# Optimization experiments

Measured on AMD Instinct MI355X. Metric: run time of the kernel, lower is better.

The kernel has to match this reference:

```python
import jax, jax.numpy as jnp
import numpy as np

N, DIM, T, V = 32, 256, 120, 25
H, HD = 8, 32            # num_heads, head_dim
MAX_HOP = 4
SCALE = HD ** -0.5


def setup_inputs() -> dict:
    key = jax.random.key(0)
    ks = jax.random.split(key, 9)
    x = jax.random.normal(ks[0], (N, DIM, T, V), jnp.float32)
    e = jax.random.normal(ks[1], (N, DIM, T, V), jnp.float32)
    # 1x1 conv weights (trunc_normal std=0.02 in the original init)
    W_kv = jax.random.normal(ks[2], (2 * DIM, DIM), jnp.float32) * 0.02
    W_q = jax.random.normal(ks[3], (DIM, DIM), jnp.float32) * 0.02
    W_proj = jax.random.normal(ks[4], (DIM, DIM), jnp.float32) * 0.02
    b_proj = jnp.zeros((DIM,), jnp.float32)
    rpe = jax.random.normal(ks[5], (MAX_HOP + 1, DIM), jnp.float32) * 0.02
    w1 = jax.random.normal(ks[6], (H, HD), jnp.float32) * 0.02
    # outer initialized as per-head identity (plus noise so grads are interesting)
    outer = jnp.broadcast_to(jnp.eye(V, dtype=jnp.float32), (H, V, V)) \
        + 0.1 * jax.random.normal(ks[7], (H, V, V), jnp.float32)
    alpha = 0.1 * jax.random.normal(ks[8], (1,), jnp.float32)
    idx = jnp.arange(V)
    hops = jnp.minimum(jnp.abs(idx[:, None] - idx[None, :]), MAX_HOP).astype(jnp.int32)
    return dict(x=x, e=e, W_kv=W_kv, W_q=W_q, W_proj=W_proj, b_proj=b_proj,
                rpe=rpe, w1=w1, outer=outer, alpha=alpha, hops=hops)


def reference(x, e, W_kv, W_q, W_proj, b_proj, rpe, w1, outer, alpha, hops):
    n, c, t, v = x.shape
    # 1x1 convs == channel matmuls
    kv = jnp.einsum('nctv,dc->ndtv', x, W_kv)                    # [N,2*DIM,T,V]
    kv = kv.reshape(n, 2, H, HD, t, v).transpose(1, 0, 4, 2, 5, 3)  # [2,N,T,H,V,HD]
    k, vv = kv[0], kv[1]
    q = jnp.einsum('nctv,dc->ndtv', x, W_q)
    q = q.reshape(n, H, HD, t, v).transpose(0, 3, 1, 4, 2)       # [N,T,H,V,HD]
    # content score
    attn = jnp.einsum('bthnc,bthmc->bthnm', q, k)                # [N,T,H,V,V]
    # hop relative-position bias
    k_r = rpe[hops].reshape(v, v, H, HD)                         # [V,V,H,HD]
    attn = attn + jnp.einsum('bthnc,nmhc->bthnm', q, k_r)
    # group term
    e_k = e.reshape(n, H, HD, t, v).transpose(0, 3, 1, 4, 2)     # [N,T,H,V,HD]
    attn = attn + jnp.einsum('bthnc,bthmc->bthnm', q, e_k)
    # group bias (broadcast over query index)
    attn = attn + jnp.einsum('hc,bthmc->bthm', w1, e_k)[..., None, :]
    attn = jax.nn.softmax(attn * SCALE, axis=-1)
    # outer/adjacency fusion then weighted V
    out = jnp.einsum('bthnm,bthmc->bthnc', alpha[0] * attn + outer, vv)
    # [N,T,H,V,HD] -> [N,T,H,HD,V] -> [N,T,DIM,V] -> [N,DIM,T,V]
    out = out.transpose(0, 1, 2, 4, 3).reshape(n, t, H * HD, v).transpose(0, 2, 1, 3)
    out = jnp.einsum('nctv,dc->ndtv', out, W_proj) + b_proj[None, :, None, None]
    return out
```

## Files before the change

### kernel.cpp

```cpp
#include <hip/hip_runtime.h>

typedef __attribute__((ext_vector_type(8))) short bf16x8;
typedef __attribute__((ext_vector_type(4))) float f32x4;
typedef unsigned short u16;
typedef unsigned int u32;

#define SCALE_ 0.17677669529663687f
#define MFMA(a,b,c) __builtin_amdgcn_mfma_f32_16x16x32_bf16(a,b,c,0,0,0)

__device__ __forceinline__ u16 f2bf(float f){
    u32 u = __float_as_uint(f);
    u = (u + 0x7FFFu + ((u >> 16) & 1u)) >> 16;
    return (u16)u;
}
__device__ __forceinline__ float bf2f(u32 h){ return __uint_as_float(h << 16); }
__device__ __forceinline__ u32 pk2(float a, float b){ return (u32)f2bf(a) | ((u32)f2bf(b) << 16); }

__device__ __forceinline__ bf16x8 frag8(uint2 p0, uint2 p1, int kg, int l15){
    const int s0 = ((kg & 1) << 5) + l15;
    const int s1 = s0 + 16;
    u32 a0 = (u32)__shfl((int)p0.x, s0, 64);
    u32 a1 = (u32)__shfl((int)p0.y, s0, 64);
    u32 a2 = (u32)__shfl((int)p0.x, s1, 64);
    u32 a3 = (u32)__shfl((int)p0.y, s1, 64);
    u32 b0 = (u32)__shfl((int)p1.x, s0, 64);
    u32 b1 = (u32)__shfl((int)p1.y, s0, 64);
    u32 b2 = (u32)__shfl((int)p1.x, s1, 64);
    u32 b3 = (u32)__shfl((int)p1.y, s1, 64);
    const bool hi = (kg >= 2);
    union { u32 u[4]; bf16x8 v; } r;
    r.u[0] = hi ? b0 : a0; r.u[1] = hi ? b1 : a1;
    r.u[2] = hi ? b2 : a2; r.u[3] = hi ? b3 : a3;
    return r.v;
}

#define O_OFF_ 263680
__global__ void prep_kernel(const float* __restrict__ Wkv, const float* __restrict__ Wq,
                            const float* __restrict__ Wproj, const float* __restrict__ rpe,
                            const float* __restrict__ w1, u16* __restrict__ wpk)
{
    int i = blockIdx.x * 256 + threadIdx.x;
    if (i < 65536)        wpk[i] = f2bf(Wq[i]);
    else if (i < 131072)  wpk[i] = f2bf(Wkv[i - 65536]);
    else if (i < 196608){
        int j = i - 131072;
        int h = j >> 13;
        int r = j & 8191;
        int coct = r >> 8;
        int hd   = (r >> 3) & 31;
        int clo  = r & 7;
        wpk[i] = f2bf(Wkv[(size_t)(256 + h*32 + hd) * 256 + coct*8 + clo]);
    }
    else if (i < 262144)  wpk[i] = f2bf(Wproj[i - 196608]);
    else if (i < 263424){
        int j = i - 262144;
        int jj = j >> 8, h = (j >> 5) & 7, hd = j & 31;
        wpk[i] = f2bf(rpe[jj*256 + h*32 + hd]);
    }
    else if (i < 263680)  wpk[i] = f2bf(w1[i - 263424]);
}

__launch_bounds__(512)
__global__ void attn_kernel(const float* __restrict__ x, const float* __restrict__ e,
                            const float* __restrict__ outer, const float* __restrict__ alpha,
                            const u16* __restrict__ wpk, u16* __restrict__ o_ws)
{
    __shared__ __align__(16) u16 smem[6656*2 + 64];
    u16* xs  = smem;
    u16* es  = smem + 6656;

    const int tid = threadIdx.x;
    const int w = tid >> 6, lane = tid & 63;
    const int l15 = lane & 15, kg = lane >> 4;
    const int wg = (blockIdx.x & 7) * 480 + (blockIdx.x >> 3);
    const int n = wg / 120, t = wg % 120;
    const float alpha0 = alpha[0];
    const f32x4 zf = {0.f, 0.f, 0.f, 0.f};

    const float* xb = x + (size_t)n*768000 + t*25;
    const float* eb = e + (size_t)n*768000 + t*25;
    for (int i = tid; i < 6400; i += 512){
        int c = i / 25, v = i - c*25;
        int a16 = ((c>>3)*26 + v)*8 + (c&7);
        xs[a16] = f2bf(xb[c*3000 + v]);
        es[a16] = f2bf(eb[c*3000 + v]);
    }
    __syncthreads();

    const int h = w;

    f32x4 cq[2][2], ck[2][2];
    #pragma unroll
    for (int i = 0; i < 2; ++i)
        #pragma unroll
        for (int j = 0; j < 2; ++j){ cq[i][j] = zf; ck[i][j] = zf; }
    {
        const u16* wq0 = wpk + (size_t)(h*32 + l15)*256;
        const u16* wk0 = wpk + 65536 + (size_t)(h*32 + l15)*256;
        #pragma unroll
        for (int ks = 0; ks < 8; ++ks){
            bf16x8 b0 = *(const bf16x8*)&xs[((ks*4+kg)*26 + l15)*8];
            bf16x8 b1 = *(const bf16x8*)&xs[((ks*4+kg)*26 + 16 + l15)*8];
            bf16x8 aq0 = *(const bf16x8*)(wq0 + ks*32 + kg*8);
            bf16x8 aq1 = *(const bf16x8*)(wq0 + 4096 + ks*32 + kg*8);
            bf16x8 ak0 = *(const bf16x8*)(wk0 + ks*32 + kg*8);
            bf16x8 ak1 = *(const bf16x8*)(wk0 + 4096 + ks*32 + kg*8);
            cq[0][0]=MFMA(aq0,b0,cq[0][0]); cq[0][1]=MFMA(aq0,b1,cq[0][1]);
            cq[1][0]=MFMA(aq1,b0,cq[1][0]); cq[1][1]=MFMA(aq1,b1,cq[1][1]);
            ck[0][0]=MFMA(ak0,b0,ck[0][0]); ck[0][1]=MFMA(ak0,b1,ck[0][1]);
            ck[1][0]=MFMA(ak1,b0,ck[1][0]); ck[1][1]=MFMA(ak1,b1,ck[1][1]);
        }
    }
    uint2 P_q[2][2], P_k[2][2];
    #pragma unroll
    for (int mt = 0; mt < 2; ++mt)
        #pragma unroll
        for (int nt = 0; nt < 2; ++nt){
            int coct = h*4 + mt*2 + (kg>>1);
            uint2 ev = *(const uint2*)&es[(coct*26 + nt*16 + l15)*8 + (kg&1)*4];
            ck[mt][nt][0] += bf2f(ev.x & 0xFFFFu);
            ck[mt][nt][1] += bf2f(ev.x >> 16);
            ck[mt][nt][2] += bf2f(ev.y & 0xFFFFu);
            ck[mt][nt][3] += bf2f(ev.y >> 16);
            uint2 pq; pq.x = pk2(cq[mt][nt][0], cq[mt][nt][1]);
            pq.y = pk2(cq[mt][nt][2], cq[mt][nt][3]);
            P_q[nt][mt] = pq;
            uint2 pk; pk.x = pk2(ck[mt][nt][0], ck[mt][nt][1]);
            pk.y = pk2(ck[mt][nt][2], ck[mt][nt][3]);
            P_k[nt][mt] = pk;
        }

    float bias01[2];
    {
        bf16x8 aw1 = *(const bf16x8*)(wpk + 263424 + h*32 + kg*8);
        bf16x8 be0 = *(const bf16x8*)&es[((h*4+kg)*26 + l15)*8];
        bf16x8 be1 = *(const bf16x8*)&es[((h*4+kg)*26 + 16 + l15)*8];
        f32x4 cb0 = MFMA(aw1, be0, zf);
        f32x4 cb1 = MFMA(aw1, be1, zf);
        bias01[0] = cb0[0]; bias01[1] = cb1[0];
    }

    f32x4 cv[2][2];
    #pragma unroll
    for (int i = 0; i < 2; ++i)
        #pragma unroll
        for (int j = 0; j < 2; ++j) cv[i][j] = zf;
    {
        const u16* wvt = wpk + 131072 + h*8192;
        #pragma unroll
        for (int ks = 0; ks < 8; ++ks){
            bf16x8 a0 = *(const bf16x8*)&xs[((ks*4+kg)*26 + l15)*8];
            bf16x8 a1 = *(const bf16x8*)&xs[((ks*4+kg)*26 + 16 + l15)*8];
            bf16x8 bv0 = *(const bf16x8*)&wvt[((ks*4+kg)*32 + l15)*8];
            bf16x8 bv1 = *(const bf16x8*)&wvt[((ks*4+kg)*32 + 16 + l15)*8];
            cv[0][0]=MFMA(a0,bv0,cv[0][0]); cv[0][1]=MFMA(a0,bv1,cv[0][1]);
            cv[1][0]=MFMA(a1,bv0,cv[1][0]); cv[1][1]=MFMA(a1,bv1,cv[1][1]);
        }
    }
    #pragma unroll
    for (int nt = 0; nt < 2; ++nt)
        #pragma unroll
        for (int r = 0; r < 4; ++r)
            cv[1][nt][r] = (kg*4 + r < 9) ? cv[1][nt][r] : 0.f;

    uint2 P_v[2][2];
    #pragma unroll
    for (int mt = 0; mt < 2; ++mt)
        #pragma unroll
        for (int nt = 0; nt < 2; ++nt){
            uint2 pv; pv.x = pk2(cv[mt][nt][0], cv[mt][nt][1]);
            pv.y = pk2(cv[mt][nt][2], cv[mt][nt][3]);
            P_v[nt][mt] = pv;
        }

    bf16x8 fq0  = frag8(P_q[0][0], P_q[0][1], kg, l15);
    bf16x8 fq1  = frag8(P_q[1][0], P_q[1][1], kg, l15);
    bf16x8 fke0 = frag8(P_k[0][0], P_k[0][1], kg, l15);
    bf16x8 fke1 = frag8(P_k[1][0], P_k[1][1], kg, l15);
    if (l15 >= 9){
        if (l15 <= 13)
            fke1 = *(const bf16x8*)(wpk + 262144 + ((l15-9)*8 + h)*32 + kg*8);
        else {
            union { u32 u[4]; bf16x8 v; } z; z.u[0]=z.u[1]=z.u[2]=z.u[3]=0;
            fke1 = z.v;
        }
    }
    f32x4 sc[2][2];
    sc[0][0] = MFMA(fke0, fq0, zf);
    sc[0][1] = MFMA(fke0, fq1, zf);
    sc[1][0] = MFMA(fke1, fq0, zf);
    sc[1][1] = MFMA(fke1, fq1, zf);

    uint2 P_G[2][2];
    #pragma unroll
    for (int nt = 0; nt < 2; ++nt){
        const int a = nt*16 + l15;
        f32x4 s0 = sc[0][nt], s1 = sc[1][nt];
        float rr0 = __shfl(s1[1], 32 + l15, 64);
        float rr1 = __shfl(s1[2], 32 + l15, 64);
        float rr2 = __shfl(s1[3], 32 + l15, 64);
        float rr3 = __shfl(s1[0], 48 + l15, 64);
        float rr4 = __shfl(s1[1], 48 + l15, 64);
        float tv[8];
        #pragma unroll
        for (int mt = 0; mt < 2; ++mt)
            #pragma unroll
            for (int r = 0; r < 4; ++r){
                int b = mt*16 + kg*4 + r;
                float sval = mt ? s1[r] : s0[r];
                float bb = __shfl(bias01[mt], (lane & 48) + (b & 15), 64);
                int d = a - b; d = d < 0 ? -d : d; if (d > 4) d = 4;
                float rj = d==0?rr0 : d==1?rr1 : d==2?rr2 : d==3?rr3 : rr4;
                float tt = (sval + rj + bb) * SCALE_;
                tv[mt*4+r] = (b < 25) ? tt : -1e30f;
            }
        float m = tv[0];
        #pragma unroll
        for (int i = 1; i < 8; ++i) m = fmaxf(m, tv[i]);
        m = fmaxf(m, __shfl_xor(m, 16, 64));
        m = fmaxf(m, __shfl_xor(m, 32, 64));
        float ex[8], sm = 0.f;
        #pragma unroll
        for (int i = 0; i < 8; ++i){ ex[i] = __expf(tv[i] - m); sm += ex[i]; }
        sm += __shfl_xor(sm, 16, 64);
        sm += __shfl_xor(sm, 32, 64);
        const float inv = alpha0 / sm;
        float g[8];
        #pragma unroll
        for (int mt = 0; mt < 2; ++mt)
            #pragma unroll
            for (int r = 0; r < 4; ++r){
                int b = mt*16 + kg*4 + r;
                float ov = (a < 25 && b < 25) ? outer[((size_t)h*25 + a)*25 + b] : 0.f;
                g[mt*4+r] = (b < 25) ? ex[mt*4+r]*inv + ov : 0.f;
            }
        uint2 pg0; pg0.x = pk2(g[0], g[1]); pg0.y = pk2(g[2], g[3]);
        uint2 pg1; pg1.x = pk2(g[4], g[5]); pg1.y = pk2(g[6], g[7]);
        P_G[nt][0] = pg0; P_G[nt][1] = pg1;
    }

    {
        bf16x8 fv0 = frag8(P_v[0][0], P_v[0][1], kg, l15);
        bf16x8 fv1 = frag8(P_v[1][0], P_v[1][1], kg, l15);
        bf16x8 fg0 = frag8(P_G[0][0], P_G[0][1], kg, l15);
        bf16x8 fg1 = frag8(P_G[1][0], P_G[1][1], kg, l15);
        f32x4 o[2][2];
        o[0][0] = MFMA(fv0, fg0, zf); o[0][1] = MFMA(fv0, fg1, zf);
        o[1][0] = MFMA(fv1, fg0, zf); o[1][1] = MFMA(fv1, fg1, zf);
        u16* od = o_ws + (size_t)wg * 6400;
        #pragma unroll
        for (int mt = 0; mt < 2; ++mt)
            #pragma unroll
            for (int nt = 0; nt < 2; ++nt){
                int a = nt*16 + l15;
                if (a < 25){
                    int coct = h*4 + mt*2 + (kg>>1);
                    u32* dst = (u32*)&od[(coct*25 + a)*8 + (kg&1)*4];
                    dst[0] = pk2(o[mt][nt][0], o[mt][nt][1]);
                    dst[1] = pk2(o[mt][nt][2], o[mt][nt][3]);
                }
            }
    }
}

__launch_bounds__(512)
__global__ void proj_kernel(const u16* __restrict__ wpk, const u16* __restrict__ o_ws,
                            const float* __restrict__ bproj, float* __restrict__ out)
{
    const int tid = threadIdx.x;
    const int w = tid >> 6, lane = tid & 63;
    const int l15 = lane & 15, kg = lane >> 4;
    const int wg = (blockIdx.x & 7) * 480 + (blockIdx.x >> 3);
    const int n = wg / 120, t = wg % 120;
    const f32x4 zf = {0.f, 0.f, 0.f, 0.f};
    const u16* ob = o_ws + (size_t)wg * 6400;

    f32x4 pc[2][2];
    #pragma unroll
    for (int i = 0; i < 2; ++i){ pc[i][0] = zf; pc[i][1] = zf; }
    #pragma unroll
    for (int ks = 0; ks < 8; ++ks){
        bf16x8 pb0 = *(const bf16x8*)&ob[((ks*4+kg)*25 + l15)*8];
        bf16x8 pb1 = *(const bf16x8*)&ob[((ks*4+kg)*25 + 16 + l15)*8];
        #pragma unroll
        for (int i = 0; i < 2; ++i){
            bf16x8 aw = *(const bf16x8*)(wpk + 196608 +
                            (size_t)(w*32 + i*16 + l15)*256 + ks*32 + kg*8);
            pc[i][0] = MFMA(aw, pb0, pc[i][0]);
            pc[i][1] = MFMA(aw, pb1, pc[i][1]);
        }
    }
    #pragma unroll
    for (int i = 0; i < 2; ++i){
        const int d = w*32 + i*16 + kg*4;
        float b0 = bproj[d], b1 = bproj[d+1], b2 = bproj[d+2], b3 = bproj[d+3];
        #pragma unroll
        for (int nt = 0; nt < 2; ++nt){
            int v = nt*16 + l15;
            if (v < 25){
                float* op = out + (size_t)n*768000 + (size_t)d*3000 + t*25 + v;
                op[0]    = pc[i][nt][0] + b0;
                op[3000] = pc[i][nt][1] + b1;
                op[6000] = pc[i][nt][2] + b2;
                op[9000] = pc[i][nt][3] + b3;
            }
        }
    }
}

__launch_bounds__(512, 4)
__global__ void mhsa_main(const float* __restrict__ x, const float* __restrict__ e,
                          const float* __restrict__ outer, const float* __restrict__ alpha,
                          const float* __restrict__ bproj, const u16* __restrict__ wpk,
                          float* __restrict__ out)
{
    __shared__ __align__(16) u16 smem[6656*3 + 64];
    u16* xs  = smem;
    u16* es  = smem + 6656;
    u16* opk = smem + 13312;

    const int tid = threadIdx.x;
    const int w = tid >> 6, lane = tid & 63;
    const int l15 = lane & 15, kg = lane >> 4;
    const int wg = (blockIdx.x & 7) * 480 + (blockIdx.x >> 3);
    const int n = wg / 120, t = wg % 120;
    const float alpha0 = alpha[0];
    const f32x4 zf = {0.f, 0.f, 0.f, 0.f};

    const float* xb = x + (size_t)n*768000 + t*25;
    const float* eb = e + (size_t)n*768000 + t*25;
    for (int i = tid; i < 6400; i += 512){
        int c = i / 25, v = i - c*25;
        int a16 = ((c>>3)*26 + v)*8 + (c&7);
        xs[a16] = f2bf(xb[c*3000 + v]);
        es[a16] = f2bf(eb[c*3000 + v]);
    }
    __syncthreads();

    {
        const int h = w;
        f32x4 cq[2][2], ck[2][2];
        #pragma unroll
        for (int i = 0; i < 2; ++i)
            #pragma unroll
            for (int j = 0; j < 2; ++j){ cq[i][j] = zf; ck[i][j] = zf; }
        {
            const u16* wq0 = wpk + (size_t)(h*32 + l15)*256;
            const u16* wk0 = wpk + 65536 + (size_t)(h*32 + l15)*256;
            #pragma unroll
            for (int ks = 0; ks < 8; ++ks){
                bf16x8 b0 = *(const bf16x8*)&xs[((ks*4+kg)*26 + l15)*8];
                bf16x8 b1 = *(const bf16x8*)&xs[((ks*4+kg)*26 + 16 + l15)*8];
                bf16x8 aq0 = *(const bf16x8*)(wq0 + ks*32 + kg*8);
                bf16x8 aq1 = *(const bf16x8*)(wq0 + 4096 + ks*32 + kg*8);
                bf16x8 ak0 = *(const bf16x8*)(wk0 + ks*32 + kg*8);
                bf16x8 ak1 = *(const bf16x8*)(wk0 + 4096 + ks*32 + kg*8);
                cq[0][0]=MFMA(aq0,b0,cq[0][0]); cq[0][1]=MFMA(aq0,b1,cq[0][1]);
                cq[1][0]=MFMA(aq1,b0,cq[1][0]); cq[1][1]=MFMA(aq1,b1,cq[1][1]);
                ck[0][0]=MFMA(ak0,b0,ck[0][0]); ck[0][1]=MFMA(ak0,b1,ck[0][1]);
                ck[1][0]=MFMA(ak1,b0,ck[1][0]); ck[1][1]=MFMA(ak1,b1,ck[1][1]);
            }
        }
        uint2 P_q[2][2], P_k[2][2];
        #pragma unroll
        for (int mt = 0; mt < 2; ++mt)
            #pragma unroll
            for (int nt = 0; nt < 2; ++nt){
                int coct = h*4 + mt*2 + (kg>>1);
                uint2 ev = *(const uint2*)&es[(coct*26 + nt*16 + l15)*8 + (kg&1)*4];
                ck[mt][nt][0] += bf2f(ev.x & 0xFFFFu);
                ck[mt][nt][1] += bf2f(ev.x >> 16);
                ck[mt][nt][2] += bf2f(ev.y & 0xFFFFu);
                ck[mt][nt][3] += bf2f(ev.y >> 16);
                uint2 pq; pq.x = pk2(cq[mt][nt][0], cq[mt][nt][1]);
                pq.y = pk2(cq[mt][nt][2], cq[mt][nt][3]);
                P_q[nt][mt] = pq;
                uint2 pk; pk.x = pk2(ck[mt][nt][0], ck[mt][nt][1]);
                pk.y = pk2(ck[mt][nt][2], ck[mt][nt][3]);
                P_k[nt][mt] = pk;
            }
        float bias01[2];
        {
            bf16x8 aw1 = *(const bf16x8*)(wpk + 263424 + h*32 + kg*8);
            bf16x8 be0 = *(const bf16x8*)&es[((h*4+kg)*26 + l15)*8];
            bf16x8 be1 = *(const bf16x8*)&es[((h*4+kg)*26 + 16 + l15)*8];
            f32x4 cb0 = MFMA(aw1, be0, zf);
            f32x4 cb1 = MFMA(aw1, be1, zf);
            bias01[0] = cb0[0]; bias01[1] = cb1[0];
        }
        f32x4 cv[2][2];
        #pragma unroll
        for (int i = 0; i < 2; ++i)
            #pragma unroll
            for (int j = 0; j < 2; ++j) cv[i][j] = zf;
        {
            const u16* wvt = wpk + 131072 + h*8192;
            #pragma unroll
            for (int ks = 0; ks < 8; ++ks){
                bf16x8 a0 = *(const bf16x8*)&xs[((ks*4+kg)*26 + l15)*8];
                bf16x8 a1 = *(const bf16x8*)&xs[((ks*4+kg)*26 + 16 + l15)*8];
                bf16x8 bv0 = *(const bf16x8*)&wvt[((ks*4+kg)*32 + l15)*8];
                bf16x8 bv1 = *(const bf16x8*)&wvt[((ks*4+kg)*32 + 16 + l15)*8];
                cv[0][0]=MFMA(a0,bv0,cv[0][0]); cv[0][1]=MFMA(a0,bv1,cv[0][1]);
                cv[1][0]=MFMA(a1,bv0,cv[1][0]); cv[1][1]=MFMA(a1,bv1,cv[1][1]);
            }
        }
        #pragma unroll
        for (int nt = 0; nt < 2; ++nt)
            #pragma unroll
            for (int r = 0; r < 4; ++r)
                cv[1][nt][r] = (kg*4 + r < 9) ? cv[1][nt][r] : 0.f;
        uint2 P_v[2][2];
        #pragma unroll
        for (int mt = 0; mt < 2; ++mt)
            #pragma unroll
            for (int nt = 0; nt < 2; ++nt){
                uint2 pv; pv.x = pk2(cv[mt][nt][0], cv[mt][nt][1]);
                pv.y = pk2(cv[mt][nt][2], cv[mt][nt][3]);
                P_v[nt][mt] = pv;
            }
        bf16x8 fq0  = frag8(P_q[0][0], P_q[0][1], kg, l15);
        bf16x8 fq1  = frag8(P_q[1][0], P_q[1][1], kg, l15);
        bf16x8 fke0 = frag8(P_k[0][0], P_k[0][1], kg, l15);
        bf16x8 fke1 = frag8(P_k[1][0], P_k[1][1], kg, l15);
        if (l15 >= 9){
            if (l15 <= 13)
                fke1 = *(const bf16x8*)(wpk + 262144 + ((l15-9)*8 + h)*32 + kg*8);
            else {
                union { u32 u[4]; bf16x8 v; } z; z.u[0]=z.u[1]=z.u[2]=z.u[3]=0;
                fke1 = z.v;
            }
        }
        f32x4 sc[2][2];
        sc[0][0] = MFMA(fke0, fq0, zf);
        sc[0][1] = MFMA(fke0, fq1, zf);
        sc[1][0] = MFMA(fke1, fq0, zf);
        sc[1][1] = MFMA(fke1, fq1, zf);
        uint2 P_G[2][2];
        #pragma unroll
        for (int nt = 0; nt < 2; ++nt){
            const int a = nt*16 + l15;
            f32x4 s0 = sc[0][nt], s1 = sc[1][nt];
            float rr0 = __shfl(s1[1], 32 + l15, 64);
            float rr1 = __shfl(s1[2], 32 + l15, 64);
            float rr2 = __shfl(s1[3], 32 + l15, 64);
            float rr3 = __shfl(s1[0], 48 + l15, 64);
            float rr4 = __shfl(s1[1], 48 + l15, 64);
            float tv[8];
            #pragma unroll
            for (int mt = 0; mt < 2; ++mt)
                #pragma unroll
                for (int r = 0; r < 4; ++r){
                    int b = mt*16 + kg*4 + r;
                    float sval = mt ? s1[r] : s0[r];
                    float bb = __shfl(bias01[mt], (lane & 48) + (b & 15), 64);
                    int d = a - b; d = d < 0 ? -d : d; if (d > 4) d = 4;
                    float rj = d==0?rr0 : d==1?rr1 : d==2?rr2 : d==3?rr3 : rr4;
                    float tt = (sval + rj + bb) * SCALE_;
                    tv[mt*4+r] = (b < 25) ? tt : -1e30f;
                }
            float m = tv[0];
            #pragma unroll
            for (int i = 1; i < 8; ++i) m = fmaxf(m, tv[i]);
            m = fmaxf(m, __shfl_xor(m, 16, 64));
            m = fmaxf(m, __shfl_xor(m, 32, 64));
            float ex[8], sm = 0.f;
            #pragma unroll
            for (int i = 0; i < 8; ++i){ ex[i] = __expf(tv[i] - m); sm += ex[i]; }
            sm += __shfl_xor(sm, 16, 64);
            sm += __shfl_xor(sm, 32, 64);
            const float inv = alpha0 / sm;
            float g[8];
            #pragma unroll
            for (int mt = 0; mt < 2; ++mt)
                #pragma unroll
                for (int r = 0; r < 4; ++r){
                    int b = mt*16 + kg*4 + r;
                    float ov = (a < 25 && b < 25) ? outer[((size_t)h*25 + a)*25 + b] : 0.f;
                    g[mt*4+r] = (b < 25) ? ex[mt*4+r]*inv + ov : 0.f;
                }
            uint2 pg0; pg0.x = pk2(g[0], g[1]); pg0.y = pk2(g[2], g[3]);
            uint2 pg1; pg1.x = pk2(g[4], g[5]); pg1.y = pk2(g[6], g[7]);
            P_G[nt][0] = pg0; P_G[nt][1] = pg1;
        }
        {
            bf16x8 fv0 = frag8(P_v[0][0], P_v[0][1], kg, l15);
            bf16x8 fv1 = frag8(P_v[1][0], P_v[1][1], kg, l15);
            bf16x8 fg0 = frag8(P_G[0][0], P_G[0][1], kg, l15);
            bf16x8 fg1 = frag8(P_G[1][0], P_G[1][1], kg, l15);
            f32x4 o[2][2];
            o[0][0] = MFMA(fv0, fg0, zf); o[0][1] = MFMA(fv0, fg1, zf);
            o[1][0] = MFMA(fv1, fg0, zf); o[1][1] = MFMA(fv1, fg1, zf);
            #pragma unroll
            for (int mt = 0; mt < 2; ++mt)
                #pragma unroll
                for (int nt = 0; nt < 2; ++nt){
                    int a = nt*16 + l15;
                    if (a < 25){
                        int coct = h*4 + mt*2 + (kg>>1);
                        u32* dst = (u32*)&opk[(coct*26 + a)*8 + (kg&1)*4];
                        dst[0] = pk2(o[mt][nt][0], o[mt][nt][1]);
                        dst[1] = pk2(o[mt][nt][2], o[mt][nt][3]);
                    }
                }
        }
    }
    __syncthreads();

    {
        f32x4 pc[2][2];
        #pragma unroll
        for (int i = 0; i < 2; ++i){ pc[i][0] = zf; pc[i][1] = zf; }
        #pragma unroll
        for (int ks = 0; ks < 8; ++ks){
            bf16x8 pb0 = *(const bf16x8*)&opk[((ks*4+kg)*26 + l15)*8];
            bf16x8 pb1 = *(const bf16x8*)&opk[((ks*4+kg)*26 + 16 + l15)*8];
            #pragma unroll
            for (int i = 0; i < 2; ++i){
                bf16x8 aw = *(const bf16x8*)(wpk + 196608 +
                                (size_t)(w*32 + i*16 + l15)*256 + ks*32 + kg*8);
                pc[i][0] = MFMA(aw, pb0, pc[i][0]);
                pc[i][1] = MFMA(aw, pb1, pc[i][1]);
            }
        }
        #pragma unroll
        for (int i = 0; i < 2; ++i){
            const int d = w*32 + i*16 + kg*4;
            float b0 = bproj[d], b1 = bproj[d+1], b2 = bproj[d+2], b3 = bproj[d+3];
            #pragma unroll
            for (int nt = 0; nt < 2; ++nt){
                int v = nt*16 + l15;
                if (v < 25){
                    float* op = out + (size_t)n*768000 + (size_t)d*3000 + t*25 + v;
                    op[0]    = pc[i][nt][0] + b0;
                    op[3000] = pc[i][nt][1] + b1;
                    op[6000] = pc[i][nt][2] + b2;
                    op[9000] = pc[i][nt][3] + b3;
                }
            }
        }
    }
}

extern "C" void kernel_launch(void* const* d_in, const int* in_sizes, int n_in,
                              void* d_out, int out_size, void* d_ws, size_t ws_size,
                              hipStream_t stream) {
    (void)in_sizes; (void)n_in; (void)out_size;
    const float* x     = (const float*)d_in[0];
    const float* e     = (const float*)d_in[1];
    const float* Wkv   = (const float*)d_in[2];
    const float* Wq    = (const float*)d_in[3];
    const float* Wproj = (const float*)d_in[4];
    const float* bproj = (const float*)d_in[5];
    const float* rpe   = (const float*)d_in[6];
    const float* w1    = (const float*)d_in[7];
    const float* outer = (const float*)d_in[8];
    const float* alpha = (const float*)d_in[9];
    float* out = (float*)d_out;
    u16* wpk = (u16*)d_ws;

    prep_kernel<<<1030, 256, 0, stream>>>(Wkv, Wq, Wproj, rpe, w1, wpk);

    const size_t need = (size_t)O_OFF_*2 + (size_t)3840*6400*2 + 4096;
    if (ws_size >= need){
        u16* o_ws = wpk + O_OFF_;
        attn_kernel<<<32*120, 512, 0, stream>>>(x, e, outer, alpha, wpk, o_ws);
        proj_kernel<<<32*120, 512, 0, stream>>>(wpk, o_ws, bproj, out);
    } else {
        mhsa_main<<<32*120, 512, 0, stream>>>(x, e, outer, alpha, bproj, wpk, out);
    }
}
```

Measured before the change: 315.2 us.

## Split QKV projection into a batched GEMM kernel and fuse attention with output projection

Moves the Q, K and V 1x1-conv projections into a separate GEMM kernel. Each block handles one projection section over four time steps (100 columns), so weight fragments are reused across more columns and x and e are loaded with float4 reads. The result is written as per-(n,t,head) bf16 pages already laid out as MFMA fragments, plus a precomputed group-bias buffer. Attention and the output projection are fused into one kernel through shared memory, replacing the old global o_ws round trip. The cost is extra global traffic for the Q/K/V pages and the bias buffer, and a larger workspace requirement.

```diff
diff --git a/kernel.cpp b/kernel.cpp
--- a/kernel.cpp
+++ b/kernel.cpp
@@ -34,23 +34,17 @@
     return r.v;
 }
 
-#define O_OFF_ 263680
+#define PG_OFF_ 333312
+#define NPAGES_ ((size_t)3840*8*2624)
+#define BIAS_U16_ (PG_OFF_ + NPAGES_)
+
 __global__ void prep_kernel(const float* __restrict__ Wkv, const float* __restrict__ Wq,
                             const float* __restrict__ Wproj, const float* __restrict__ rpe,
                             const float* __restrict__ w1, u16* __restrict__ wpk)
 {
     int i = blockIdx.x * 256 + threadIdx.x;
     if (i < 65536)        wpk[i] = f2bf(Wq[i]);
-    else if (i < 131072)  wpk[i] = f2bf(Wkv[i - 65536]);
-    else if (i < 196608){
-        int j = i - 131072;
-        int h = j >> 13;
-        int r = j & 8191;
-        int coct = r >> 8;
-        int hd   = (r >> 3) & 31;
-        int clo  = r & 7;
-        wpk[i] = f2bf(Wkv[(size_t)(256 + h*32 + hd) * 256 + coct*8 + clo]);
-    }
+    else if (i < 196608)  wpk[i] = f2bf(Wkv[i - 65536]);
     else if (i < 262144)  wpk[i] = f2bf(Wproj[i - 196608]);
     else if (i < 263424){
         int j = i - 262144;
@@ -58,138 +52,184 @@
         wpk[i] = f2bf(rpe[jj*256 + h*32 + hd]);
     }
     else if (i < 263680)  wpk[i] = f2bf(w1[i - 263424]);
+    else if (i < 267776){
+        int j = i - 263680;
+        int r = j >> 8, c = j & 255;
+        float v = (r < 8 && (c >> 5) == r) ? w1[r*32 + (c & 31)] : 0.f;
+        wpk[i] = f2bf(v);
+    }
+    else if (i < 333312){
+        int j = i - 267776;
+        int h = j >> 13;
+        int r = j & 8191;
+        int coct = r >> 8, hd = (r >> 3) & 31, clo = r & 7;
+        wpk[i] = f2bf(Wkv[(size_t)(256 + h*32 + hd) * 256 + coct*8 + clo]);
+    }
 }
 
 __launch_bounds__(512)
-__global__ void attn_kernel(const float* __restrict__ x, const float* __restrict__ e,
-                            const float* __restrict__ outer, const float* __restrict__ alpha,
-                            const u16* __restrict__ wpk, u16* __restrict__ o_ws)
+__global__ void qkv_gemm(const float* __restrict__ x, const float* __restrict__ e,
+                         const u16* __restrict__ wpk, u16* __restrict__ pages,
+                         float* __restrict__ bias_ws)
 {
-    __shared__ __align__(16) u16 smem[6656*2 + 64];
-    u16* xs  = smem;
-    u16* es  = smem + 6656;
+    __shared__ __align__(16) u16 xt[25664];
 
     const int tid = threadIdx.x;
     const int w = tid >> 6, lane = tid & 63;
     const int l15 = lane & 15, kg = lane >> 4;
-    const int wg = (blockIdx.x & 7) * 480 + (blockIdx.x >> 3);
+    const int wg = ((int)blockIdx.x & 7) * 360 + ((int)blockIdx.x >> 3);
+    const int sec = wg / 960, cb = wg % 960;
+    const int n = cb / 30, tg = cb % 30;
+    const f32x4 zf = {0.f, 0.f, 0.f, 0.f};
+
+    const float* xb = x + (size_t)n*768000 + tg*100;
+    for (int i = tid; i < 6400; i += 512){
+        int c = i / 25, c4 = i - c*25;
+        float4 v4 = *(const float4*)&xb[c*3000 + c4*4];
+        int base = ((c>>3)*100 + c4*4)*8 + (c&7);
+        xt[base]    = f2bf(v4.x);
+        xt[base+8]  = f2bf(v4.y);
+        xt[base+16] = f2bf(v4.z);
+        xt[base+24] = f2bf(v4.w);
+    }
+    __syncthreads();
+
+    f32x4 acc[2][8];
+    #pragma unroll
+    for (int m = 0; m < 2; ++m)
+        #pragma unroll
+        for (int f = 0; f < 8; ++f) acc[m][f] = zf;
+
+    const u16* wrow = wpk + (size_t)(sec*256 + w*32 + l15) * 256;
+    #pragma unroll
+    for (int ks = 0; ks < 8; ++ks){
+        bf16x8 a0 = *(const bf16x8*)(wrow + ks*32 + kg*8);
+        bf16x8 a1 = *(const bf16x8*)(wrow + 4096 + ks*32 + kg*8);
+        #pragma unroll
+        for (int f = 0; f < 8; ++f){
+            int col = (f>>1)*25 + (f&1)*16 + l15;
+            bf16x8 b = *(const bf16x8*)&xt[((ks*4+kg)*100 + col)*8];
+            acc[0][f] = MFMA(a0, b, acc[0][f]);
+            acc[1][f] = MFMA(a1, b, acc[1][f]);
+        }
+    }
+
+    if (sec == 1){
+        __syncthreads();
+        const float* ebp = e + (size_t)n*768000 + tg*100;
+        for (int i = tid; i < 6400; i += 512){
+            int c = i / 25, c4 = i - c*25;
+            float4 v4 = *(const float4*)&ebp[c*3000 + c4*4];
+            int base = ((c>>3)*100 + c4*4)*8 + (c&7);
+            xt[base]    = f2bf(v4.x);
+            xt[base+8]  = f2bf(v4.y);
+            xt[base+16] = f2bf(v4.z);
+            xt[base+24] = f2bf(v4.w);
+        }
+        __syncthreads();
+        #pragma unroll
+        for (int m = 0; m < 2; ++m){
+            int c0 = w*32 + m*16 + kg*4;
+            #pragma unroll
+            for (int f = 0; f < 8; ++f){
+                int col = (f>>1)*25 + (f&1)*16 + l15;
+                uint2 ev = *(const uint2*)&xt[((c0>>3)*100 + col)*8 + (c0&7)];
+                acc[m][f][0] += bf2f(ev.x & 0xFFFFu);
+                acc[m][f][1] += bf2f(ev.x >> 16);
+                acc[m][f][2] += bf2f(ev.y & 0xFFFFu);
+                acc[m][f][3] += bf2f(ev.y >> 16);
+            }
+        }
+    }
+
+    const int secoff = (sec == 0) ? 0 : (sec == 1 ? 800 : 1600);
+    #pragma unroll
+    for (int m = 0; m < 2; ++m){
+        #pragma unroll
+        for (int f = 0; f < 8; ++f){
+            int tt = f >> 1, a = (f&1)*16 + l15;
+            if (a < 25){
+                size_t nt = (size_t)(n*120 + tg*4 + tt);
+                u16* pg = pages + (nt*8 + w)*2624 + secoff;
+                int hd0 = m*16 + kg*4;
+                if (sec < 2){
+                    uint2 val; val.x = pk2(acc[m][f][0], acc[m][f][1]);
+                    val.y = pk2(acc[m][f][2], acc[m][f][3]);
+                    *(uint2*)&pg[((hd0>>3)*25 + a)*8 + (hd0&7)] = val;
+                } else {
+                    #pragma unroll
+                    for (int r = 0; r < 4; ++r)
+                        pg[((a>>3)*32 + hd0 + r)*8 + (a&7)] = f2bf(acc[m][f][r]);
+                }
+            }
+        }
+    }
+
+    if (sec == 1 && w == 0){
+        f32x4 bacc[8];
+        #pragma unroll
+        for (int f = 0; f < 8; ++f) bacc[f] = zf;
+        const u16* w1f = wpk + 263680 + l15*256;
+        #pragma unroll
+        for (int ks = 0; ks < 8; ++ks){
+            bf16x8 a = *(const bf16x8*)(w1f + ks*32 + kg*8);
+            #pragma unroll
+            for (int f = 0; f < 8; ++f){
+                int col = (f>>1)*25 + (f&1)*16 + l15;
+                bf16x8 b = *(const bf16x8*)&xt[((ks*4+kg)*100 + col)*8];
+                bacc[f] = MFMA(a, b, bacc[f]);
+            }
+        }
+        if (kg < 2){
+            #pragma unroll
+            for (int f = 0; f < 8; ++f){
+                int tt = f >> 1, a = (f&1)*16 + l15;
+                if (a < 25){
+                    int nt = n*120 + tg*4 + tt;
+                    #pragma unroll
+                    for (int r = 0; r < 4; ++r)
+                        bias_ws[(size_t)nt*256 + (kg*4+r)*32 + a] = bacc[f][r];
+                }
+            }
+        }
+    }
+}
+
+__launch_bounds__(512)
+__global__ void attn_proj(const float* __restrict__ outer, const float* __restrict__ alpha,
+                          const float* __restrict__ bproj, const u16* __restrict__ wpk,
+                          const u16* __restrict__ pages, const float* __restrict__ bias_ws,
+                          float* __restrict__ out)
+{
+    __shared__ __align__(16) u16 opk[6656 + 64];
+
+    const int tid = threadIdx.x;
+    const int w = tid >> 6, lane = tid & 63;
+    const int l15 = lane & 15, kg = lane >> 4;
+    const int wg = ((int)blockIdx.x & 7) * 480 + ((int)blockIdx.x >> 3);
     const int n = wg / 120, t = wg % 120;
     const float alpha0 = alpha[0];
     const f32x4 zf = {0.f, 0.f, 0.f, 0.f};
-
-    const float* xb = x + (size_t)n*768000 + t*25;
-    const float* eb = e + (size_t)n*768000 + t*25;
-    for (int i = tid; i < 6400; i += 512){
-        int c = i / 25, v = i - c*25;
-        int a16 = ((c>>3)*26 + v)*8 + (c&7);
-        xs[a16] = f2bf(xb[c*3000 + v]);
-        es[a16] = f2bf(eb[c*3000 + v]);
-    }
-    __syncthreads();
-
     const int h = w;
-
-    f32x4 cq[2][2], ck[2][2];
-    #pragma unroll
-    for (int i = 0; i < 2; ++i)
-        #pragma unroll
-        for (int j = 0; j < 2; ++j){ cq[i][j] = zf; ck[i][j] = zf; }
-    {
-        const u16* wq0 = wpk + (size_t)(h*32 + l15)*256;
-        const u16* wk0 = wpk + 65536 + (size_t)(h*32 + l15)*256;
-        #pragma unroll
-        for (int ks = 0; ks < 8; ++ks){
-            bf16x8 b0 = *(const bf16x8*)&xs[((ks*4+kg)*26 + l15)*8];
-            bf16x8 b1 = *(const bf16x8*)&xs[((ks*4+kg)*26 + 16 + l15)*8];
-            bf16x8 aq0 = *(const bf16x8*)(wq0 + ks*32 + kg*8);
-            bf16x8 aq1 = *(const bf16x8*)(wq0 + 4096 + ks*32 + kg*8);
-            bf16x8 ak0 = *(const bf16x8*)(wk0 + ks*32 + kg*8);
-            bf16x8 ak1 = *(const bf16x8*)(wk0 + 4096 + ks*32 + kg*8);
-            cq[0][0]=MFMA(aq0,b0,cq[0][0]); cq[0][1]=MFMA(aq0,b1,cq[0][1]);
-            cq[1][0]=MFMA(aq1,b0,cq[1][0]); cq[1][1]=MFMA(aq1,b1,cq[1][1]);
-            ck[0][0]=MFMA(ak0,b0,ck[0][0]); ck[0][1]=MFMA(ak0,b1,ck[0][1]);
-            ck[1][0]=MFMA(ak1,b0,ck[1][0]); ck[1][1]=MFMA(ak1,b1,ck[1][1]);
-        }
-    }
-    uint2 P_q[2][2], P_k[2][2];
-    #pragma unroll
-    for (int mt = 0; mt < 2; ++mt)
-        #pragma unroll
-        for (int nt = 0; nt < 2; ++nt){
-            int coct = h*4 + mt*2 + (kg>>1);
-            uint2 ev = *(const uint2*)&es[(coct*26 + nt*16 + l15)*8 + (kg&1)*4];
-            ck[mt][nt][0] += bf2f(ev.x & 0xFFFFu);
-            ck[mt][nt][1] += bf2f(ev.x >> 16);
-            ck[mt][nt][2] += bf2f(ev.y & 0xFFFFu);
-            ck[mt][nt][3] += bf2f(ev.y >> 16);
-            uint2 pq; pq.x = pk2(cq[mt][nt][0], cq[mt][nt][1]);
-            pq.y = pk2(cq[mt][nt][2], cq[mt][nt][3]);
-            P_q[nt][mt] = pq;
-            uint2 pk; pk.x = pk2(ck[mt][nt][0], ck[mt][nt][1]);
-            pk.y = pk2(ck[mt][nt][2], ck[mt][nt][3]);
-            P_k[nt][mt] = pk;
-        }
-
-    float bias01[2];
-    {
-        bf16x8 aw1 = *(const bf16x8*)(wpk + 263424 + h*32 + kg*8);
-        bf16x8 be0 = *(const bf16x8*)&es[((h*4+kg)*26 + l15)*8];
-        bf16x8 be1 = *(const bf16x8*)&es[((h*4+kg)*26 + 16 + l15)*8];
-        f32x4 cb0 = MFMA(aw1, be0, zf);
-        f32x4 cb1 = MFMA(aw1, be1, zf);
-        bias01[0] = cb0[0]; bias01[1] = cb1[0];
-    }
-
-    f32x4 cv[2][2];
-    #pragma unroll
-    for (int i = 0; i < 2; ++i)
-        #pragma unroll
-        for (int j = 0; j < 2; ++j) cv[i][j] = zf;
-    {
-        const u16* wvt = wpk + 131072 + h*8192;
-        #pragma unroll
-        for (int ks = 0; ks < 8; ++ks){
-            bf16x8 a0 = *(const bf16x8*)&xs[((ks*4+kg)*26 + l15)*8];
-            bf16x8 a1 = *(const bf16x8*)&xs[((ks*4+kg)*26 + 16 + l15)*8];
-            bf16x8 bv0 = *(const bf16x8*)&wvt[((ks*4+kg)*32 + l15)*8];
-            bf16x8 bv1 = *(const bf16x8*)&wvt[((ks*4+kg)*32 + 16 + l15)*8];
-            cv[0][0]=MFMA(a0,bv0,cv[0][0]); cv[0][1]=MFMA(a0,bv1,cv[0][1]);
-            cv[1][0]=MFMA(a1,bv0,cv[1][0]); cv[1][1]=MFMA(a1,bv1,cv[1][1]);
-        }
-    }
-    #pragma unroll
-    for (int nt = 0; nt < 2; ++nt)
-        #pragma unroll
-        for (int r = 0; r < 4; ++r)
-            cv[1][nt][r] = (kg*4 + r < 9) ? cv[1][nt][r] : 0.f;
-
-    uint2 P_v[2][2];
-    #pragma unroll
-    for (int mt = 0; mt < 2; ++mt)
-        #pragma unroll
-        for (int nt = 0; nt < 2; ++nt){
-            uint2 pv; pv.x = pk2(cv[mt][nt][0], cv[mt][nt][1]);
-            pv.y = pk2(cv[mt][nt][2], cv[mt][nt][3]);
-            P_v[nt][mt] = pv;
-        }
-
-    bf16x8 fq0  = frag8(P_q[0][0], P_q[0][1], kg, l15);
-    bf16x8 fq1  = frag8(P_q[1][0], P_q[1][1], kg, l15);
-    bf16x8 fke0 = frag8(P_k[0][0], P_k[0][1], kg, l15);
-    bf16x8 fke1 = frag8(P_k[1][0], P_k[1][1], kg, l15);
-    if (l15 >= 9){
-        if (l15 <= 13)
-            fke1 = *(const bf16x8*)(wpk + 262144 + ((l15-9)*8 + h)*32 + kg*8);
-        else {
-            union { u32 u[4]; bf16x8 v; } z; z.u[0]=z.u[1]=z.u[2]=z.u[3]=0;
-            fke1 = z.v;
-        }
-    }
+    const u16* pg = pages + ((size_t)wg*8 + h)*2624;
+
+    bf16x8 fq0  = *(const bf16x8*)&pg[(kg*25 + l15)*8];
+    bf16x8 fq1  = *(const bf16x8*)&pg[(kg*25 + 16 + l15)*8];
+    bf16x8 fke0 = *(const bf16x8*)&pg[800 + (kg*25 + l15)*8];
+    bf16x8 fke1;
+    if (l15 < 9)       fke1 = *(const bf16x8*)&pg[800 + (kg*25 + 16 + l15)*8];
+    else if (l15 <= 13) fke1 = *(const bf16x8*)(wpk + 262144 + ((l15-9)*8 + h)*32 + kg*8);
+    else { union { u32 u[4]; bf16x8 v; } z; z.u[0]=z.u[1]=z.u[2]=z.u[3]=0; fke1 = z.v; }
+
     f32x4 sc[2][2];
     sc[0][0] = MFMA(fke0, fq0, zf);
     sc[0][1] = MFMA(fke0, fq1, zf);
     sc[1][0] = MFMA(fke1, fq0, zf);
     sc[1][1] = MFMA(fke1, fq1, zf);
+
+    float bias01[2];
+    bias01[0] = bias_ws[(size_t)wg*256 + h*32 + l15];
+    bias01[1] = bias_ws[(size_t)wg*256 + h*32 + 16 + l15];
 
     uint2 P_G[2][2];
     #pragma unroll
@@ -240,14 +280,13 @@
     }
 
     {
-        bf16x8 fv0 = frag8(P_v[0][0], P_v[0][1], kg, l15);
-        bf16x8 fv1 = frag8(P_v[1][0], P_v[1][1], kg, l15);
+        bf16x8 fv0 = *(const bf16x8*)&pg[1600 + (kg*32 + l15)*8];
+        bf16x8 fv1 = *(const bf16x8*)&pg[1600 + (kg*32 + 16 + l15)*8];
         bf16x8 fg0 = frag8(P_G[0][0], P_G[0][1], kg, l15);
         bf16x8 fg1 = frag8(P_G[1][0], P_G[1][1], kg, l15);
         f32x4 o[2][2];
         o[0][0] = MFMA(fv0, fg0, zf); o[0][1] = MFMA(fv0, fg1, zf);
         o[1][0] = MFMA(fv1, fg0, zf); o[1][1] = MFMA(fv1, fg1, zf);
-        u16* od = o_ws + (size_t)wg * 6400;
         #pragma unroll
         for (int mt = 0; mt < 2; ++mt)
             #pragma unroll
@@ -255,54 +294,44 @@
                 int a = nt*16 + l15;
                 if (a < 25){
                     int coct = h*4 + mt*2 + (kg>>1);
-                    u32* dst = (u32*)&od[(coct*25 + a)*8 + (kg&1)*4];
+                    u32* dst = (u32*)&opk[(coct*26 + a)*8 + (kg&1)*4];
                     dst[0] = pk2(o[mt][nt][0], o[mt][nt][1]);
                     dst[1] = pk2(o[mt][nt][2], o[mt][nt][3]);
                 }
             }
     }
-}
-
-__launch_bounds__(512)
-__global__ void proj_kernel(const u16* __restrict__ wpk, const u16* __restrict__ o_ws,
-                            const float* __restrict__ bproj, float* __restrict__ out)
-{
-    const int tid = threadIdx.x;
-    const int w = tid >> 6, lane = tid & 63;
-    const int l15 = lane & 15, kg = lane >> 4;
-    const int wg = (blockIdx.x & 7) * 480 + (blockIdx.x >> 3);
-    const int n = wg / 120, t = wg % 120;
-    const f32x4 zf = {0.f, 0.f, 0.f, 0.f};
-    const u16* ob = o_ws + (size_t)wg * 6400;
-
-    f32x4 pc[2][2];
-    #pragma unroll
-    for (int i = 0; i < 2; ++i){ pc[i][0] = zf; pc[i][1] = zf; }
-    #pragma unroll
-    for (int ks = 0; ks < 8; ++ks){
-        bf16x8 pb0 = *(const bf16x8*)&ob[((ks*4+kg)*25 + l15)*8];
-        bf16x8 pb1 = *(const bf16x8*)&ob[((ks*4+kg)*25 + 16 + l15)*8];
+    __syncthreads();
+
+    {
+        f32x4 pc[2][2];
+        #pragma unroll
+        for (int i = 0; i < 2; ++i){ pc[i][0] = zf; pc[i][1] = zf; }
+        #pragma unroll
+        for (int ks = 0; ks < 8; ++ks){
+            bf16x8 pb0 = *(const bf16x8*)&opk[((ks*4+kg)*26 + l15)*8];
+            bf16x8 pb1 = *(const bf16x8*)&opk[((ks*4+kg)*26 + 16 + l15)*8];
+            #pragma unroll
+            for (int i = 0; i < 2; ++i){
+                bf16x8 aw = *(const bf16x8*)(wpk + 196608 +
+                                (size_t)(w*32 + i*16 + l15)*256 + ks*32 + kg*8);
+                pc[i][0] = MFMA(aw, pb0, pc[i][0]);
+                pc[i][1] = MFMA(aw, pb1, pc[i][1]);
+            }
+        }
         #pragma unroll
         for (int i = 0; i < 2; ++i){
-            bf16x8 aw = *(const bf16x8*)(wpk + 196608 +
-                            (size_t)(w*32 + i*16 + l15)*256 + ks*32 + kg*8);
-            pc[i][0] = MFMA(aw, pb0, pc[i][0]);
-            pc[i][1] = MFMA(aw, pb1, pc[i][1]);
-        }
-    }
-    #pragma unroll
-    for (int i = 0; i < 2; ++i){
-        const int d = w*32 + i*16 + kg*4;
-        float b0 = bproj[d], b1 = bproj[d+1], b2 = bproj[d+2], b3 = bproj[d+3];
-        #pragma unroll
-        for (int nt = 0; nt < 2; ++nt){
-            int v = nt*16 + l15;
-            if (v < 25){
-                float* op = out + (size_t)n*768000 + (size_t)d*3000 + t*25 + v;
-                op[0]    = pc[i][nt][0] + b0;
-                op[3000] = pc[i][nt][1] + b1;
-                op[6000] = pc[i][nt][2] + b2;
-                op[9000] = pc[i][nt][3] + b3;
+            const int d = w*32 + i*16 + kg*4;
+            float b0 = bproj[d], b1 = bproj[d+1], b2 = bproj[d+2], b3 = bproj[d+3];
+            #pragma unroll
+            for (int nt = 0; nt < 2; ++nt){
+                int v = nt*16 + l15;
+                if (v < 25){
+                    float* op = out + (size_t)n*768000 + (size_t)d*3000 + t*25 + v;
+                    op[0]    = pc[i][nt][0] + b0;
+                    op[3000] = pc[i][nt][1] + b1;
+                    op[6000] = pc[i][nt][2] + b2;
+                    op[9000] = pc[i][nt][3] + b3;
+                }
             }
         }
     }
@@ -394,7 +423,7 @@
             #pragma unroll
             for (int j = 0; j < 2; ++j) cv[i][j] = zf;
         {
-            const u16* wvt = wpk + 131072 + h*8192;
+            const u16* wvt = wpk + 267776 + h*8192;
             #pragma unroll
             for (int ks = 0; ks < 8; ++ks){
                 bf16x8 a0 = *(const bf16x8*)&xs[((ks*4+kg)*26 + l15)*8];
@@ -559,14 +588,15 @@
     float* out = (float*)d_out;
     u16* wpk = (u16*)d_ws;
 
-    prep_kernel<<<1030, 256, 0, stream>>>(Wkv, Wq, Wproj, rpe, w1, wpk);
-
-    const size_t need = (size_t)O_OFF_*2 + (size_t)3840*6400*2 + 4096;
+    prep_kernel<<<1302, 256, 0, stream>>>(Wkv, Wq, Wproj, rpe, w1, wpk);
+
+    const size_t need = (size_t)BIAS_U16_ * 2 + (size_t)3840*256*4 + 4096;
     if (ws_size >= need){
-        u16* o_ws = wpk + O_OFF_;
-        attn_kernel<<<32*120, 512, 0, stream>>>(x, e, outer, alpha, wpk, o_ws);
-        proj_kernel<<<32*120, 512, 0, stream>>>(wpk, o_ws, bproj, out);
+        u16* pages = wpk + PG_OFF_;
+        float* bias_ws = (float*)(wpk + BIAS_U16_);
+        qkv_gemm<<<2880, 512, 0, stream>>>(x, e, wpk, pages, bias_ws);
+        attn_proj<<<3840, 512, 0, stream>>>(outer, alpha, bproj, wpk, pages, bias_ws, out);
     } else {
-        mhsa_main<<<32*120, 512, 0, stream>>>(x, e, outer, alpha, bproj, wpk, out);
+        mhsa_main<<<3840, 512, 0, stream>>>(x, e, outer, alpha, bproj, wpk, out);
     }
 }
```

After: 311.1 us. No clear change (-1.3%).
